# Performance work log

Measured on AMD Instinct MI355X. Metric: run time of the kernel, lower is better.

Reference implementation:

```python
import jax, jax.numpy as jnp
import numpy as np

B, S, D, H = 2, 2048, 1024, 16
DK = D // H

def setup_inputs() -> dict:
    key = jax.random.key(0)
    ks = jax.random.split(key, 12)
    s = 1.0 / np.sqrt(D)
    inp = {
        'q': jax.random.normal(ks[0], (B, S, D), jnp.float32),
        'k': jax.random.normal(ks[1], (B, S, D), jnp.float32),
        'v': jax.random.normal(ks[2], (B, S, D), jnp.float32),
        'mask': jnp.tril(jnp.ones((S, S), jnp.int32))[None, None],  # [1,1,S,S] causal
        'Wq': jax.random.normal(ks[3], (D, D), jnp.float32) * s,
        'bq': jax.random.normal(ks[4], (D,), jnp.float32) * s,
        'Wk': jax.random.normal(ks[5], (D, D), jnp.float32) * s,
        'bk': jax.random.normal(ks[6], (D,), jnp.float32) * s,
        'Wv': jax.random.normal(ks[7], (D, D), jnp.float32) * s,
        'bv': jax.random.normal(ks[8], (D,), jnp.float32) * s,
        'Wo': jax.random.normal(ks[9], (D, D), jnp.float32) * s,
        'bo': jax.random.normal(ks[10], (D,), jnp.float32) * s,
    }
    return inp

def reference(q, k, v, mask, Wq, bq, Wk, bk, Wv, bv, Wo, bo):
    # linear projections (torch nn.Linear: x @ W.T + b)
    query = q @ Wq.T + bq
    key_ = k @ Wk.T + bk
    value = v @ Wv.T + bv
    # [B,S,D] -> [B,H,S,dk]
    def split_heads(x):
        return x.reshape(B, S, H, DK).transpose(0, 2, 1, 3)
    query, key_, value = split_heads(query), split_heads(key_), split_heads(value)
    scores = jnp.einsum('bhqd,bhkd->bhqk', query, key_) / jnp.sqrt(jnp.float32(DK))
    scores = jnp.where(mask == 0, jnp.float32(-1e9), scores)
    # FAITHFUL to source: softmax over dim=1 (the HEAD axis), not dim=-1
    attn = jax.nn.softmax(scores, axis=1)
    x = jnp.einsum('bhqk,bhkd->bhqd', attn, value)
    x = x.transpose(0, 2, 1, 3).reshape(B, S, D)
    return x @ Wo.T + bo
```

## Files before the change

### kernel.cpp

```cpp
#include <hip/hip_runtime.h>
#include <hip/hip_bf16.h>
#include <stdint.h>
#include <stddef.h>


typedef __attribute__((ext_vector_type(8))) __bf16 bf16x8;
typedef __attribute__((ext_vector_type(4))) __bf16 bf16x4;
typedef __attribute__((ext_vector_type(2))) _Float16 f16x2;
typedef __attribute__((ext_vector_type(4))) _Float16 f16x4;
typedef __attribute__((ext_vector_type(8))) _Float16 f16x8;
typedef __attribute__((ext_vector_type(4))) float  f32x4;
typedef __attribute__((ext_vector_type(8))) float  f32x8;

#define MFMA_BF16_K32(a,b,c) __builtin_amdgcn_mfma_f32_16x16x32_bf16((a),(b),(c),0,0,0)
#define MFMA_F16_K16(a,b,c)  __builtin_amdgcn_mfma_f32_16x16x16f16((a),(b),(c),0,0,0)
#define MFMA_FP8_K32(a,b,c) \
  __builtin_amdgcn_mfma_f32_16x16x32_fp8_fp8((long long)(a),(long long)(b),(c),0,0,0)

template <typename T> __device__ inline f32x8 ld8(const T* p);
template <> __device__ inline f32x8 ld8<float>(const float* p) { return *(const f32x8*)p; }
template <> __device__ inline f32x8 ld8<__bf16>(const __bf16* p) {
  return __builtin_convertvector(*(const bf16x8*)p, f32x8);
}

__device__ __forceinline__ void gl_lds16(const __bf16* g, __bf16* l) {
  __builtin_amdgcn_global_load_lds(
      (const __attribute__((address_space(1))) void*)g,
      (__attribute__((address_space(3))) void*)l, 16, 0, 0);
}

__device__ __forceinline__ f16x2 pk2(float a, float b) {
  return __builtin_bit_cast(f16x2, __builtin_amdgcn_cvt_pkrtz(a, b));
}

__device__ __forceinline__ unsigned char to_fp8(float v) {
  return (unsigned char)(__builtin_amdgcn_cvt_pk_fp8_f32(v, v, 0, false) & 0xFF);
}
__device__ __forceinline__ float from_fp8(unsigned char b8) {
  return __builtin_amdgcn_cvt_f32_fp8((int)b8, 0);
}

__device__ __forceinline__ int permd(int d) {
  return ((d >> 3) & 3) * 16 + (d >> 5) * 8 + (d & 7);
}

__device__ __forceinline__ void epi_store(int mode, float val, int m, int n, void* dst) {
  if (mode == 0) {
    ((float*)dst)[(size_t)m * 1024 + n] = val;
  } else if (mode == 4) {
    const int bb = m >> 11, s = m & 2047, h = n >> 6, d = n & 63;
    ((unsigned char*)dst)[((size_t)(h * 2) + bb) * 131072 + s * 64 + permd(d)] = to_fp8(val);
  } else if (mode == 5) {
    const int bb = m >> 11, s = m & 2047, h = n >> 6, d = n & 63;
    unsigned char* p0 = (unsigned char*)dst + ((size_t)(h * 2) + bb) * 262144 + (size_t)s * 128;
    const unsigned char hi = to_fp8(val);
    p0[permd(d)]      = hi;
    p0[64 + permd(d)] = to_fp8((val - from_fp8(hi)) * 16.f);
  } else {
    const int bb = m >> 11, s = m & 2047, h = n >> 6, d = n & 63;
    ((_Float16*)dst)[((((size_t)bb * 128 + (s >> 4)) * 16 + h) * 64 + d) * 16 + (s & 15)] =
        (_Float16)val;
  }
}

struct CvtArgs { const float* src[7]; __bf16* dst[7]; };

__global__ __launch_bounds__(256) void cvt_kernel(CvtArgs a, int nqkv, int nw) {
  const int t = blockIdx.y;
  const int n = (t < 3) ? nqkv : nw;
  const int base = (blockIdx.x * 256 + threadIdx.x) * 8;
  if (base >= n) return;
  *(bf16x8*)(a.dst[t] + base) =
      __builtin_convertvector(*(const f32x8*)(a.src[t] + base), bf16x8);
}

struct GemmSet {
  const __bf16* A0[3]; const __bf16* A1[3]; const __bf16* A2[3]; const __bf16* A3[3];
  const __bf16* W[3]; const float* bias[3]; void* dst[3]; int mode[3];
};

__global__ __launch_bounds__(256) void gemm_tile(GemmSet g) {
  const int z = blockIdx.z;
  const __bf16* __restrict__ A0 = g.A0[z];
  const __bf16* __restrict__ A1 = g.A1[z];
  const __bf16* __restrict__ A2 = g.A2[z];
  const __bf16* __restrict__ A3 = g.A3[z];
  const __bf16* __restrict__ W  = g.W[z];
  const float*  __restrict__ bias = g.bias[z];
  void* dst = g.dst[z];
  const int mode = g.mode[z];

  __shared__ __bf16 sh[2][128 * 64];
  __bf16* As = sh[0];
  __bf16* Bs = sh[1];
  const int tid  = threadIdx.x;
  const int lane = tid & 63, wid = tid >> 6;
  const int l15  = lane & 15, quad = lane >> 4;
  const int m0   = blockIdx.y * 128;
  const int n0   = blockIdx.x * 128;
  const int srow = lane >> 3;
  const int swz  = ((lane & 7) ^ srow) * 8;
  const int wm   = (wid >> 1) * 64;
  const int wn   = (wid & 1) * 64;
  const int mr = tid >> 3;
  const int mc = tid & 7;
  const int mg = ((mc ^ (mr & 7)) * 8);

  f32x4 acc[4][4] = {};

  for (int k0 = 0; k0 < 1024; k0 += 64) {
    if (A1 != nullptr) {
      #pragma unroll
      for (int gI = 0; gI < 4; ++gI) {
        const size_t gi = (size_t)(m0 + gI * 32 + mr) * 1024 + k0 + mg;
        f32x8 s = ld8(&A0[gi]) + ld8(&A1[gi]) + ld8(&A2[gi]) + ld8(&A3[gi]);
        *(bf16x8*)&As[(gI * 32 + mr) * 64 + mc * 8] = __builtin_convertvector(s, bf16x8);
      }
    } else {
      #pragma unroll
      for (int i = 0; i < 4; ++i)
        gl_lds16(A0 + (size_t)(m0 + wid * 32 + i * 8 + srow) * 1024 + k0 + swz,
                 &As[(wid * 32 + i * 8) * 64]);
    }
    #pragma unroll
    for (int i = 0; i < 4; ++i)
      gl_lds16(W + (size_t)(n0 + wid * 32 + i * 8 + srow) * 1024 + k0 + swz,
               &Bs[(wid * 32 + i * 8) * 64]);
    __syncthreads();
    #pragma unroll
    for (int kk = 0; kk < 64; kk += 32) {
      const int slot = (((kk >> 3) + quad) ^ (l15 & 7)) * 8;
      bf16x8 fa[4], fb[4];
      #pragma unroll
      for (int ms = 0; ms < 4; ++ms)
        fa[ms] = *(const bf16x8*)&As[(wm + ms * 16 + l15) * 64 + slot];
      #pragma unroll
      for (int ns = 0; ns < 4; ++ns)
        fb[ns] = *(const bf16x8*)&Bs[(wn + ns * 16 + l15) * 64 + slot];
      #pragma unroll
      for (int ms = 0; ms < 4; ++ms)
        #pragma unroll
        for (int ns = 0; ns < 4; ++ns)
          acc[ms][ns] = MFMA_BF16_K32(fa[ms], fb[ns], acc[ms][ns]);
    }
    __syncthreads();
  }

  if (mode == 0) {
    #pragma unroll
    for (int ms = 0; ms < 4; ++ms) {
      #pragma unroll
      for (int ns = 0; ns < 4; ++ns) {
        const int n     = n0 + wn + ns * 16 + l15;
        const float bv  = bias[n];
        const int mbase = m0 + wm + ms * 16 + quad * 4;
        #pragma unroll
        for (int r = 0; r < 4; ++r)
          ((float*)dst)[(size_t)(mbase + r) * 1024 + n] = acc[ms][ns][r] + bv;
      }
    }
  } else if (mode == 4 || mode == 5) {
    const int rstride = (mode == 4) ? 64 : 128;
    char* ep = (char*)&sh[0][0] + wid * 8192;
    #pragma unroll
    for (int ms = 0; ms < 4; ++ms) {
      #pragma unroll
      for (int ns = 0; ns < 4; ++ns) {
        const int n    = n0 + wn + ns * 16 + l15;
        const float bv = bias[n];
        const int p    = permd(ns * 16 + l15);
        #pragma unroll
        for (int r = 0; r < 4; ++r) {
          const int row = ms * 16 + quad * 4 + r;
          const float v = acc[ms][ns][r] + bv;
          const unsigned char hi = to_fp8(v);
          ep[row * rstride + (p ^ ((row & 3) << 4))] = (char)hi;
          if (mode == 5)
            ep[row * rstride + ((64 + p) ^ ((row & 3) << 4))] =
                (char)to_fp8((v - from_fp8(hi)) * 16.f);
        }
      }
    }
    const int bb = (m0 + wm) >> 11;
    const int s0 = (m0 + wm) & 2047;
    const int h  = (n0 + wn) >> 6;
    unsigned char* base = (unsigned char*)dst
        + ((size_t)(h * 2) + bb) * ((mode == 4) ? 131072 : 262144);
    const int nhalf = (mode == 4) ? 1 : 2;
    for (int half = 0; half < nhalf; ++half) {
      #pragma unroll
      for (int gI = 0; gI < 4; ++gI) {
        const int row = gI * 16 + (lane >> 2);
        const int c   = lane & 3;
        uint4 val = *(const uint4*)(ep + row * rstride
                                    + ((half * 64 + c * 16) ^ ((row & 3) << 4)));
        *(uint4*)(base + (size_t)(s0 + row) * rstride + half * 64 + c * 16) = val;
      }
    }
  } else {
    char* ep = (char*)&sh[0][0] + wid * 8192;
    #pragma unroll
    for (int ms = 0; ms < 4; ++ms) {
      #pragma unroll
      for (int ns = 0; ns < 4; ++ns) {
        const int n    = n0 + wn + ns * 16 + l15;
        const float bv = bias[n];
        const int rowp = ns * 16 + l15;
        #pragma unroll
        for (int r = 0; r < 4; ++r) {
          const int colB = (ms * 16 + quad * 4 + r) * 2;
          const _Float16 hv = (_Float16)(acc[ms][ns][r] + bv);
          *(unsigned short*)(ep + rowp * 128 + (colB ^ ((rowp & 7) << 4))) =
              __builtin_bit_cast(unsigned short, hv);
        }
      }
    }
    const int bb = (m0 + wm) >> 11;
    const int s0 = (m0 + wm) & 2047;
    const int h  = (n0 + wn) >> 6;
    const int kt0 = s0 >> 4;
    #pragma unroll
    for (int dh = 0; dh < 2; ++dh) {
      const int d = dh * 32 + (lane >> 1);
      #pragma unroll
      for (int gI = 0; gI < 4; ++gI) {
        const int colB = (gI * 32 + (lane & 1) * 16) ^ ((d & 7) << 4);
        f16x8 val = *(const f16x8*)(ep + d * 128 + colB);
        _Float16* d2 = (_Float16*)dst
                       + ((size_t)(bb * 128 + kt0 + gI) * 16 + h) * 1024
                       + d * 16 + (lane & 1) * 8;
        *(f16x8*)d2 = val;
      }
    }
  }
}

template <typename TA>
__global__ __launch_bounds__(256) void gemm_bt(
    const TA* __restrict__ A0, const TA* __restrict__ A1,
    const float* __restrict__ W, const float* __restrict__ bias,
    void* dst, int mode)
{
  __shared__ __bf16 As[64][72];
  __shared__ __bf16 Bs[64][72];
  const int tid  = threadIdx.x;
  const int m0   = blockIdx.y * 64;
  const int n0   = blockIdx.x * 64;
  const int row  = tid >> 3;
  const int seg  = (tid & 7) * 8;
  const int lane = tid & 63;
  const int wid  = tid >> 6;
  const int l15  = lane & 15;
  const int quad = lane >> 4;
  const int wm   = (wid >> 1) * 32;
  const int wn   = (wid & 1) * 32;

  f32x4 acc[2][2] = {};

  for (int k0 = 0; k0 < 1024; k0 += 64) {
    const size_t i0 = (size_t)(m0 + row) * 1024 + k0 + seg;
    const size_t i1 = (size_t)(m0 + row + 32) * 1024 + k0 + seg;
    f32x8 a0 = ld8(&A0[i0]);
    f32x8 a1 = ld8(&A0[i1]);
    if (A1) { a0 += ld8(&A1[i0]); a1 += ld8(&A1[i1]); }
    f32x8 b0 = ld8(&W[(size_t)(n0 + row) * 1024 + k0 + seg]);
    f32x8 b1 = ld8(&W[(size_t)(n0 + row + 32) * 1024 + k0 + seg]);
    *(bf16x8*)&As[row][seg]      = __builtin_convertvector(a0, bf16x8);
    *(bf16x8*)&As[row + 32][seg] = __builtin_convertvector(a1, bf16x8);
    *(bf16x8*)&Bs[row][seg]      = __builtin_convertvector(b0, bf16x8);
    *(bf16x8*)&Bs[row + 32][seg] = __builtin_convertvector(b1, bf16x8);
    __syncthreads();
    #pragma unroll
    for (int kk = 0; kk < 64; kk += 32) {
      bf16x8 fa0 = *(const bf16x8*)&As[wm + l15][kk + quad * 8];
      bf16x8 fa1 = *(const bf16x8*)&As[wm + 16 + l15][kk + quad * 8];
      bf16x8 fb0 = *(const bf16x8*)&Bs[wn + l15][kk + quad * 8];
      bf16x8 fb1 = *(const bf16x8*)&Bs[wn + 16 + l15][kk + quad * 8];
      acc[0][0] = MFMA_BF16_K32(fa0, fb0, acc[0][0]);
      acc[0][1] = MFMA_BF16_K32(fa0, fb1, acc[0][1]);
      acc[1][0] = MFMA_BF16_K32(fa1, fb0, acc[1][0]);
      acc[1][1] = MFMA_BF16_K32(fa1, fb1, acc[1][1]);
    }
    __syncthreads();
  }

  #pragma unroll
  for (int ms = 0; ms < 2; ++ms) {
    #pragma unroll
    for (int ns = 0; ns < 2; ++ns) {
      const int n     = n0 + wn + ns * 16 + l15;
      const float bv  = bias[n];
      const int mbase = m0 + wm + ms * 16 + quad * 4;
      #pragma unroll
      for (int r = 0; r < 4; ++r)
        epi_store(mode, acc[ms][ns][r] + bv, mbase + r, n, dst);
    }
  }
}

__global__ __launch_bounds__(256) void tilesum_kernel(
    const _Float16* __restrict__ Vl, float* __restrict__ tsum)
{
  const int gid = blockIdx.x * 256 + threadIdx.x;
  const _Float16* p = Vl + (size_t)gid * 16;
  f32x8 s = __builtin_convertvector(*(const f16x8*)p, f32x8) +
            __builtin_convertvector(*(const f16x8*)(p + 8), f32x8);
  float tot = 0.f;
  #pragma unroll
  for (int i = 0; i < 8; ++i) tot += s[i];
  tsum[gid] = tot;
}

__global__ __launch_bounds__(64) void scan_kernel(
    const float* __restrict__ tsum, float* __restrict__ suffix)
{
  const int gid = blockIdx.x * 64 + threadIdx.x;
  const int hd = gid & 1023;
  const int b  = gid >> 10;
  const float* tp = tsum + (size_t)b * 131072 + hd;
  float* sp = suffix + (size_t)b * 131072 + hd;
  float run = 0.f;
  #pragma unroll 4
  for (int kt = 127; kt >= 0; --kt) {
    sp[(size_t)kt * 1024] = run * 0.0625f;
    run += tp[(size_t)kt * 1024];
  }
}

__global__ __launch_bounds__(256) void sufscan_kernel(
    const _Float16* __restrict__ Vl, float* __restrict__ suffix)
{
  const int gid = blockIdx.x * 256 + threadIdx.x;
  const int hd = gid & 1023;
  const int b  = gid >> 10;
  float run = 0.f;
  for (int kt = 127; kt >= 0; --kt) {
    suffix[((size_t)(b * 128 + kt)) * 1024 + hd] = run * 0.0625f;
    const _Float16* p = Vl + ((size_t)(b * 128 + kt) * 1024 + hd) * 16;
    f32x8 s = __builtin_convertvector(*(const f16x8*)p, f32x8) +
              __builtin_convertvector(*(const f16x8*)(p + 8), f32x8);
    float tot = 0.f;
    #pragma unroll
    for (int i = 0; i < 8; ++i) tot += s[i];
    run += tot;
  }
}

__global__ __launch_bounds__(256, 2) void attn_kernel(
    const unsigned char* __restrict__ Qs, const unsigned char* __restrict__ Ks,
    const _Float16* __restrict__ Vl, const float* __restrict__ suffix,
    __bf16* __restrict__ P0, __bf16* __restrict__ P1,
    __bf16* __restrict__ P2, __bf16* __restrict__ P3, int lnsl)
{
  __shared__ float Pf[2][2][4][16][20];

  const int tid   = threadIdx.x;
  const int nsl   = 1 << lnsl;
  const int b     = blockIdx.x & 1;
  const int slice = (blockIdx.x >> 1) & (nsl - 1);
  const int t     = 127 - (blockIdx.x >> (lnsl + 1));
  const int q0    = t * 16;
  const int nt    = t + 1;
  const int tbeg  = (slice * nt) >> lnsl;
  const int tend  = ((slice + 1) * nt) >> lnsl;

  const int lane = tid & 63, wid = tid >> 6;
  const int l15 = lane & 15, quad = lane >> 4;
  const float kSc   = 0.18033688011112042f;
  const float kSc16 = kSc * 0.0625f;

  ulonglong2 qhi[4], qlo[4];
  #pragma unroll
  for (int hh = 0; hh < 4; ++hh) {
    const int h = wid * 4 + hh;
    const unsigned char* qb = Qs + ((size_t)(h * 2) + b) * 262144
                              + (size_t)(q0 + l15) * 128;
    qhi[hh] = *(const ulonglong2*)(qb + quad * 16);
    qlo[hh] = *(const ulonglong2*)(qb + 64 + quad * 16);
  }

  f32x4 acc[4][4] = {};
  int buf = 0;

  for (int ct = tbeg; ct < tend; ct += 2, buf ^= 1) {
    const int ntc = (tend - ct) < 2 ? 1 : 2;
    const int cc1 = (ct + 1 < 128) ? ct + 1 : 127;
    const int ccl[2] = {ct, cc1};

    ulonglong2 kf[4][2];
    #pragma unroll
    for (int hh = 0; hh < 4; ++hh) {
      const int h = wid * 4 + hh;
      #pragma unroll
      for (int j = 0; j < 2; ++j) {
        const int krow = ccl[j] * 16 + l15;
        kf[hh][j] = *(const ulonglong2*)&Ks[((size_t)(h * 2) + b) * 131072
                                            + (size_t)krow * 64 + quad * 16];
      }
    }

    float e[4][2][4];
    float ps[2][4] = {};
    #pragma unroll
    for (int hh = 0; hh < 4; ++hh) {
      #pragma unroll
      for (int j = 0; j < 2; ++j) {
        f32x4 shi = {};
        shi = MFMA_FP8_K32(kf[hh][j].x, qhi[hh].x, shi);
        shi = MFMA_FP8_K32(kf[hh][j].y, qhi[hh].y, shi);
        f32x4 slo = {};
        slo = MFMA_FP8_K32(kf[hh][j].x, qlo[hh].x, slo);
        slo = MFMA_FP8_K32(kf[hh][j].y, qlo[hh].y, slo);
        const bool diag = (ccl[j] == t);
        #pragma unroll
        for (int r = 0; r < 4; ++r) {
          float x = shi[r] * kSc + slo[r] * kSc16;
          if (diag) x = (quad * 4 + r > l15) ? 0.f : x;
          float ev = exp2f(x);
          if (j >= ntc) ev = 0.f;
          e[hh][j][r] = ev;
          ps[j][r] += ev;
        }
      }
    }
    #pragma unroll
    for (int j = 0; j < 2; ++j) {
      f32x4 v; v[0] = ps[j][0]; v[1] = ps[j][1]; v[2] = ps[j][2]; v[3] = ps[j][3];
      *(f32x4*)&Pf[buf][j][wid][l15][quad * 4] = v;
    }

    f16x4 vf[4][2][4];
    #pragma unroll
    for (int hh = 0; hh < 4; ++hh) {
      const int h = wid * 4 + hh;
      #pragma unroll
      for (int j = 0; j < 2; ++j) {
        const _Float16* vb = Vl + ((size_t)(b * 128 + ccl[j]) * 16 + h) * 1024;
        #pragma unroll
        for (int n = 0; n < 4; ++n)
          vf[hh][j][n] = *(const f16x4*)(vb + (n * 16 + l15) * 16 + quad * 4);
      }
    }
    __syncthreads();

    float inv[2][4];
    #pragma unroll
    for (int j = 0; j < 2; ++j) {
      f32x4 tot = *(const f32x4*)&Pf[buf][j][0][l15][quad * 4];
      #pragma unroll
      for (int w = 1; w < 4; ++w)
        tot += *(const f32x4*)&Pf[buf][j][w][l15][quad * 4];
      #pragma unroll
      for (int r = 0; r < 4; ++r)
        inv[j][r] = __builtin_amdgcn_rcpf(fmaxf(tot[r], 1e-30f));
    }

    #pragma unroll
    for (int hh = 0; hh < 4; ++hh) {
      #pragma unroll
      for (int j = 0; j < 2; ++j) {
        if (j >= ntc) break;
        f16x2 lo = pk2(e[hh][j][0] * inv[j][0], e[hh][j][1] * inv[j][1]);
        f16x2 hi = pk2(e[hh][j][2] * inv[j][2], e[hh][j][3] * inv[j][3]);
        f16x4 af = __builtin_shufflevector(lo, hi, 0, 1, 2, 3);
        #pragma unroll
        for (int n = 0; n < 4; ++n)
          acc[hh][n] = MFMA_F16_K16(af, vf[hh][j][n], acc[hh][n]);
      }
    }
  }

  __bf16* Pout = slice == 0 ? P0 : slice == 1 ? P1 : slice == 2 ? P2 : P3;
  const bool last = (slice == nsl - 1);
  #pragma unroll
  for (int hh = 0; hh < 4; ++hh) {
    const int h = wid * 4 + hh;
    #pragma unroll
    for (int n = 0; n < 4; ++n) {
      const float sfx =
          last ? suffix[((size_t)(b * 128 + t)) * 1024 + h * 64 + n * 16 + l15] : 0.f;
      #pragma unroll
      for (int r = 0; r < 4; ++r)
        Pout[((size_t)(b * 2048 + q0 + quad * 4 + r)) * 1024 + h * 64 + n * 16 + l15] =
            (__bf16)(acc[hh][n][r] + sfx);
    }
  }
}

extern "C" void kernel_launch(void* const* d_in, const int* in_sizes, int n_in,
                              void* d_out, int out_size, void* d_ws, size_t ws_size,
                              hipStream_t stream) {
  const float* q  = (const float*)d_in[0];
  const float* k  = (const float*)d_in[1];
  const float* v  = (const float*)d_in[2];
  const float* Wq = (const float*)d_in[4];
  const float* bq = (const float*)d_in[5];
  const float* Wk = (const float*)d_in[6];
  const float* bk = (const float*)d_in[7];
  const float* Wv = (const float*)d_in[8];
  const float* bv = (const float*)d_in[9];
  const float* Wo = (const float*)d_in[10];
  const float* bo = (const float*)d_in[11];

  char* ws = (char*)d_ws;
  const size_t MiB = 1ull << 20;

  if (ws_size >= 67 * MiB) {
    __bf16* qc  = (__bf16*)(ws +  0 * MiB);
    __bf16* kc  = (__bf16*)(ws +  8 * MiB);
    __bf16* vc  = (__bf16*)(ws + 16 * MiB);
    __bf16* Wqc = (__bf16*)(ws + 24 * MiB);
    __bf16* Wkc = (__bf16*)(ws + 26 * MiB);
    __bf16* Wvc = (__bf16*)(ws + 28 * MiB);
    __bf16* Woc = (__bf16*)(ws + 30 * MiB);
    unsigned char* Qs = (unsigned char*)(ws + 32 * MiB);
    unsigned char* Ks = (unsigned char*)(ws + 40 * MiB);
    _Float16* Vl = (_Float16*)(ws + 48 * MiB);
    __bf16* P0  = (__bf16*)(ws + 56 * MiB);
    float* suffix = (float*)(ws + 64 * MiB);
    float* tsum   = (float*)(ws + 65 * MiB);

    CvtArgs ca;
    ca.src[0] = q;  ca.dst[0] = qc;
    ca.src[1] = k;  ca.dst[1] = kc;
    ca.src[2] = v;  ca.dst[2] = vc;
    ca.src[3] = Wq; ca.dst[3] = Wqc;
    ca.src[4] = Wk; ca.dst[4] = Wkc;
    ca.src[5] = Wv; ca.dst[5] = Wvc;
    ca.src[6] = Wo; ca.dst[6] = Woc;
    cvt_kernel<<<dim3(2048, 7), 256, 0, stream>>>(ca, 4194304, 1048576);

    GemmSet g3 = {};
    g3.A0[0] = qc; g3.W[0] = Wqc; g3.bias[0] = bq; g3.dst[0] = Qs; g3.mode[0] = 5;
    g3.A0[1] = kc; g3.W[1] = Wkc; g3.bias[1] = bk; g3.dst[1] = Ks; g3.mode[1] = 4;
    g3.A0[2] = vc; g3.W[2] = Wvc; g3.bias[2] = bv; g3.dst[2] = Vl; g3.mode[2] = 3;
    gemm_tile<<<dim3(8, 32, 3), 256, 0, stream>>>(g3);

    tilesum_kernel<<<1024, 256, 0, stream>>>(Vl, tsum);
    scan_kernel<<<32, 64, 0, stream>>>(tsum, suffix);
    attn_kernel<<<1024, 256, 0, stream>>>(Qs, Ks, Vl, suffix, P0, qc, kc, vc, 2);

    GemmSet go = {};
    go.A0[0] = P0; go.A1[0] = qc; go.A2[0] = kc; go.A3[0] = vc;
    go.W[0] = Woc; go.bias[0] = bo; go.dst[0] = d_out; go.mode[0] = 0;
    gemm_tile<<<dim3(8, 32, 1), 256, 0, stream>>>(go);
  } else {
    unsigned char* Qs = (unsigned char*)(ws);
    unsigned char* Ks = (unsigned char*)(ws + 8 * MiB);
    _Float16* Vl = (_Float16*)(ws + 16 * MiB);
    __bf16* P0  = (__bf16*)(ws + 24 * MiB);
    __bf16* P1  = (__bf16*)(ws + 32 * MiB);
    float* suffix = (float*)(ws + 40 * MiB);

    dim3 gg(16, 64, 1);
    gemm_bt<float><<<gg, 256, 0, stream>>>(q, nullptr, Wq, bq, Qs, 5);
    gemm_bt<float><<<gg, 256, 0, stream>>>(k, nullptr, Wk, bk, Ks, 4);
    gemm_bt<float><<<gg, 256, 0, stream>>>(v, nullptr, Wv, bv, Vl, 3);
    sufscan_kernel<<<8, 256, 0, stream>>>(Vl, suffix);
    attn_kernel<<<512, 256, 0, stream>>>(Qs, Ks, Vl, suffix, P0, P1, P1, P1, 1);
    gemm_bt<__bf16><<<gg, 256, 0, stream>>>(P0, P1, Wo, bo, d_out, 0);
  }
}
```

Before: 319.0 us.

## Parallelize suffix scan across 8 segments and swap GEMM grid axes

```diff
diff --git a/kernel.cpp b/kernel.cpp
--- a/kernel.cpp
+++ b/kernel.cpp
@@ -96,8 +96,8 @@
   const int tid  = threadIdx.x;
   const int lane = tid & 63, wid = tid >> 6;
   const int l15  = lane & 15, quad = lane >> 4;
-  const int m0   = blockIdx.y * 128;
-  const int n0   = blockIdx.x * 128;
+  const int m0   = blockIdx.x * 128;
+  const int n0   = blockIdx.y * 128;
   const int srow = lane >> 3;
   const int swz  = ((lane & 7) ^ srow) * 8;
   const int wm   = (wid >> 1) * 64;
@@ -311,19 +311,35 @@
   tsum[gid] = tot;
 }
 
-__global__ __launch_bounds__(64) void scan_kernel(
+__global__ __launch_bounds__(256) void scan_kernel(
     const float* __restrict__ tsum, float* __restrict__ suffix)
 {
-  const int gid = blockIdx.x * 64 + threadIdx.x;
-  const int hd = gid & 1023;
-  const int b  = gid >> 10;
+  __shared__ float gts[256];
+  const int gid = blockIdx.x * 256 + threadIdx.x;
+  const int g   = gid & 7;
+  const int hdq = gid >> 3;
+  const int hd  = hdq & 1023;
+  const int b   = hdq >> 10;
   const float* tp = tsum + (size_t)b * 131072 + hd;
+  float loc[16];
+  float gt = 0.f;
+  #pragma unroll
+  for (int i = 0; i < 16; ++i) {
+    loc[i] = tp[(size_t)(g * 16 + i) * 1024];
+    gt += loc[i];
+  }
+  gts[threadIdx.x] = gt;
+  __syncthreads();
+  const int base = threadIdx.x & ~7;
+  float run = 0.f;
+  #pragma unroll
+  for (int g2 = 0; g2 < 8; ++g2)
+    if (g2 > g) run += gts[base + g2];
   float* sp = suffix + (size_t)b * 131072 + hd;
-  float run = 0.f;
-  #pragma unroll 4
-  for (int kt = 127; kt >= 0; --kt) {
-    sp[(size_t)kt * 1024] = run * 0.0625f;
-    run += tp[(size_t)kt * 1024];
+  #pragma unroll
+  for (int i = 15; i >= 0; --i) {
+    sp[(size_t)(g * 16 + i) * 1024] = run * 0.0625f;
+    run += loc[i];
   }
 }
 
@@ -534,16 +550,16 @@
     g3.A0[0] = qc; g3.W[0] = Wqc; g3.bias[0] = bq; g3.dst[0] = Qs; g3.mode[0] = 5;
     g3.A0[1] = kc; g3.W[1] = Wkc; g3.bias[1] = bk; g3.dst[1] = Ks; g3.mode[1] = 4;
     g3.A0[2] = vc; g3.W[2] = Wvc; g3.bias[2] = bv; g3.dst[2] = Vl; g3.mode[2] = 3;
-    gemm_tile<<<dim3(8, 32, 3), 256, 0, stream>>>(g3);
+    gemm_tile<<<dim3(32, 8, 3), 256, 0, stream>>>(g3);
 
     tilesum_kernel<<<1024, 256, 0, stream>>>(Vl, tsum);
-    scan_kernel<<<32, 64, 0, stream>>>(tsum, suffix);
+    scan_kernel<<<64, 256, 0, stream>>>(tsum, suffix);
     attn_kernel<<<1024, 256, 0, stream>>>(Qs, Ks, Vl, suffix, P0, qc, kc, vc, 2);
 
     GemmSet go = {};
     go.A0[0] = P0; go.A1[0] = qc; go.A2[0] = kc; go.A3[0] = vc;
     go.W[0] = Woc; go.bias[0] = bo; go.dst[0] = d_out; go.mode[0] = 0;
-    gemm_tile<<<dim3(8, 32, 1), 256, 0, stream>>>(go);
+    gemm_tile<<<dim3(32, 8, 1), 256, 0, stream>>>(go);
   } else {
     unsigned char* Qs = (unsigned char*)(ws);
     unsigned char* Ks = (unsigned char*)(ws + 8 * MiB);
```

After: 289.1 us. 1.1x faster.
